# Kernel optimization log

Hardware: AMD Instinct MI355X
Metric: run time of the kernel (lower is better)

Reference implementation:

```python
import jax, jax.numpy as jnp
import numpy as np

IN_DIM, HIDDEN, NCLASS = 128, 512, 10
BETA, THRESH = 0.9, 0.15


def setup_inputs() -> dict:
    key = jax.random.key(0)
    k_x, k_w1, k_w2 = jax.random.split(key, 3)
    B, T = 512, 512
    x = jax.random.uniform(k_x, (B, T, IN_DIM), dtype=jnp.float32)
    # kaiming_normal_(nonlinearity='linear'): std = 1/sqrt(fan_in); fc1 then scaled by 0.8
    W1 = jax.random.normal(k_w1, (HIDDEN, IN_DIM), dtype=jnp.float32) * (0.8 / np.sqrt(IN_DIM))
    b1 = jnp.zeros((HIDDEN,), dtype=jnp.float32)
    W2 = jax.random.normal(k_w2, (NCLASS, HIDDEN), dtype=jnp.float32) * (1.0 / np.sqrt(HIDDEN))
    b2 = jnp.zeros((NCLASS,), dtype=jnp.float32)
    return {"x": x, "W1": W1, "b1": b1, "W2": W2, "b2": b2}


def reference(x, W1, b1, W2, b2):
    B, T, D = x.shape
    xs = jnp.transpose(2.0 * x, (1, 0, 2))  # [T, B, D]

    def step(carry, xt):
        mem, acc = carry
        cur = xt @ W1.T + b1                      # [B, H]
        reset = (mem > THRESH).astype(cur.dtype)  # spike from previous mem (snntorch order)
        mem = BETA * mem + cur - reset * THRESH   # subtract reset
        spk = (mem > THRESH).astype(cur.dtype)
        acc = acc + spk @ W2.T + b2               # [B, C]
        return (mem, acc), None

    mem0 = jnp.zeros((B, HIDDEN), dtype=jnp.float32)
    acc0 = jnp.zeros((B, NCLASS), dtype=jnp.float32)
    (_, acc), _ = jax.lax.scan(step, (mem0, acc0), xs)
    return acc / T
```

## Files before the change

kernel.cpp:

```cpp
#include <hip/hip_runtime.h>

#define IN_DIM  128
#define HIDDEN  512
#define NCLASS  10
#define TSTEPS  512
#define BATCH   512
#define BETA    0.9f
#define THRESH  0.15f

typedef __attribute__((ext_vector_type(8))) short bf16x8;
typedef __attribute__((ext_vector_type(4))) float f32x4;

__device__ __forceinline__ unsigned short f2bf_rne(float f) {
    unsigned int u = __float_as_uint(f);
    u += 0x7FFFu + ((u >> 16) & 1u);
    return (unsigned short)(u >> 16);
}
__device__ __forceinline__ float bf2f(unsigned short h) {
    return __uint_as_float(((unsigned int)h) << 16);
}

__device__ __forceinline__ bf16x8 cvt8(const float4 a, const float4 b, float s) {
    float v[8] = {a.x * s, a.y * s, a.z * s, a.w * s,
                  b.x * s, b.y * s, b.z * s, b.w * s};
    bf16x8 o;
#pragma unroll
    for (int e = 0; e < 8; ++e) o[e] = (short)f2bf_rne(v[e]);
    return o;
}

__device__ __forceinline__ void cvt8s(const float4 a, const float4 b,
                                      bf16x8* hi, bf16x8* lo) {
    float v[8] = {a.x, a.y, a.z, a.w, b.x, b.y, b.z, b.w};
#pragma unroll
    for (int e = 0; e < 8; ++e) {
        unsigned short h = f2bf_rne(v[e]);
        (*hi)[e] = (short)h;
        (*lo)[e] = (short)f2bf_rne(v[e] - bf2f(h));
    }
}

__global__ __launch_bounds__(256, 4) void conv_x3(
    const float* __restrict__ x, unsigned short* __restrict__ xt)
{
    const int bid  = blockIdx.x;
    const int bblk = bid >> 9;
    const int t    = bid & 511;
    const int g    = threadIdx.x;
    const int kf   = g >> 6;
    const int i    = g & 63;
    const int l15  = i & 15;
    const int lg   = i >> 4;

    const float* src = x + ((size_t)(bblk * 16 + l15) * TSTEPS + t) * IN_DIM
                         + kf * 32 + lg * 8;
    const float4* p = reinterpret_cast<const float4*>(src);
    unsigned short* tile = xt + ((size_t)bblk * TSTEPS + t) * 2048;
    *(bf16x8*)(tile + g * 8) = cvt8(p[0], p[1], 2.0f);
}

__global__ __launch_bounds__(256, 1) void snn_mfma_a(
    const unsigned short* __restrict__ xt,
    const float* __restrict__ W1, const float* __restrict__ b1,
    float* __restrict__ cnt_ws)
{
    __shared__ char ring[16][4096];

    const int bid  = blockIdx.x;
    const int hblk = bid >> 5;
    const int bblk = bid & 31;
    const int b0   = bblk * 16;
    const int tid  = threadIdx.x;
    const int wave = tid >> 6;
    const int lane = tid & 63;
    const int l15  = lane & 15;
    const int lg   = lane >> 4;
    const int hbase = hblk * 64 + wave * 16;

    bf16x8 whi[4], wlo[4];
    {
        const float* wp = W1 + (size_t)(hbase + l15) * IN_DIM + lg * 8;
#pragma unroll
        for (int kf = 0; kf < 4; ++kf) {
            const float4* p = reinterpret_cast<const float4*>(wp + kf * 32);
            cvt8s(p[0], p[1], &whi[kf], &wlo[kf]);
        }
    }
    const float b1h = b1[hbase + l15];

    const char* gb = (const char*)xt + (size_t)bblk * TSTEPS * 4096;
    char* lsb = &ring[0][0];
    const int woff   = wave * 1024;
    const int lane16 = lane * 16;
    const unsigned lbase =
        (unsigned)(unsigned long long)(__attribute__((address_space(3))) char*)&ring[0][0]
        + (unsigned)lane16;

    f32x4 mem = {0.f, 0.f, 0.f, 0.f}, cnt = {0.f, 0.f, 0.f, 0.f};

#define STAGE(TT)                                                              \
    {                                                                          \
        const char* g_ = gb + (size_t)(TT) * 4096 + woff + lane16;             \
        char* l_ = lsb + ((TT) & 15) * 4096 + woff;                            \
        __builtin_amdgcn_global_load_lds((const __attribute__((address_space(1))) void*)g_, (__attribute__((address_space(3))) void*)l_, 16, 0, 0); \
    }

#define RD1(OFF, DST)                                                          \
    asm volatile("ds_read_b128 %0, %1 offset:%c2"                              \
                 : "=&v"(DST) : "v"(lbase), "i"(OFF))

#define RD4A(S, F)                                                             \
    RD1((S) * 4096 + 0,    F[0]);                                              \
    RD1((S) * 4096 + 1024, F[1]);                                              \
    RD1((S) * 4096 + 2048, F[2]);                                              \
    RD1((S) * 4096 + 3072, F[3]);

#define MFMA_ACC(F, CH, CL)                                                    \
    CH = (f32x4){b1h, b1h, b1h, b1h};                                          \
    CL = (f32x4){0.f, 0.f, 0.f, 0.f};                                          \
    _Pragma("unroll")                                                          \
    for (int kf = 0; kf < 4; ++kf) {                                           \
        CH = __builtin_amdgcn_mfma_f32_16x16x32_bf16(F[kf], whi[kf], CH, 0, 0, 0); \
        CL = __builtin_amdgcn_mfma_f32_16x16x32_bf16(F[kf], wlo[kf], CL, 0, 0, 0); \
    }

#define REC(PH, PL)                                                            \
    _Pragma("unroll")                                                          \
    for (int r = 0; r < 4; ++r) {                                              \
        float cur = PH[r] + PL[r];                                             \
        float dec = fmaf(BETA, mem[r], cur);                                   \
        mem[r] = (mem[r] > THRESH) ? (dec - THRESH) : dec;                     \
        cnt[r] += (mem[r] > THRESH) ? 1.0f : 0.0f;                             \
    }

#define ITER_B(J, CF, NF, CH, CL, PH, PL)                                      \
    {                                                                          \
        asm volatile("s_waitcnt vmcnt(2)" ::: "memory");                       \
        __builtin_amdgcn_s_barrier();                                          \
        asm volatile("" ::: "memory");                                         \
        STAGE(tb + (J) + 7)                                                    \
        RD4A((tb + (J) + 1) & 15, NF)                                          \
        asm volatile("s_waitcnt lgkmcnt(4)" ::: "memory");                     \
        __builtin_amdgcn_sched_barrier(0);                                     \
        MFMA_ACC(CF, CH, CL)                                                   \
        REC(PH, PL)                                                            \
    }

#define ITER_N(J, CF, NF, CH, CL, PH, PL)                                      \
    {                                                                          \
        STAGE(tb + (J) + 7)                                                    \
        RD4A((tb + (J) + 1) & 15, NF)                                          \
        asm volatile("s_waitcnt lgkmcnt(4)" ::: "memory");                     \
        __builtin_amdgcn_sched_barrier(0);                                     \
        MFMA_ACC(CF, CH, CL)                                                   \
        REC(PH, PL)                                                            \
    }

    bf16x8 fA[4], fB[4];
    f32x4 hA, lA, hB, lB;
    hB = (f32x4){0.f, 0.f, 0.f, 0.f};
    lB = (f32x4){0.f, 0.f, 0.f, 0.f};

    asm volatile("s_waitcnt vmcnt(0)" ::: "memory");
#pragma unroll
    for (int j = 0; j < 7; ++j)
        STAGE(j)
    asm volatile("s_waitcnt vmcnt(6)" ::: "memory");
    __builtin_amdgcn_s_barrier();
    asm volatile("" ::: "memory");
    RD4A(0, fA)

    for (int w = 0; w < TSTEPS / 16; ++w) {
        const int tb = w * 16;
        ITER_B(0,  fA, fB, hA, lA, hB, lB)  ITER_N(1,  fB, fA, hB, lB, hA, lA)
        ITER_N(2,  fA, fB, hA, lA, hB, lB)  ITER_N(3,  fB, fA, hB, lB, hA, lA)
        ITER_B(4,  fA, fB, hA, lA, hB, lB)  ITER_N(5,  fB, fA, hB, lB, hA, lA)
        ITER_N(6,  fA, fB, hA, lA, hB, lB)  ITER_N(7,  fB, fA, hB, lB, hA, lA)
        ITER_B(8,  fA, fB, hA, lA, hB, lB)  ITER_N(9,  fB, fA, hB, lB, hA, lA)
        ITER_N(10, fA, fB, hA, lA, hB, lB)  ITER_N(11, fB, fA, hB, lB, hA, lA)
        ITER_B(12, fA, fB, hA, lA, hB, lB)  ITER_N(13, fB, fA, hB, lB, hA, lA)
        ITER_N(14, fA, fB, hA, lA, hB, lB)  ITER_N(15, fB, fA, hB, lB, hA, lA)
    }
    REC(hB, lB)
#undef ITER_B
#undef ITER_N
#undef REC
#undef MFMA_ACC
#undef RD4A
#undef RD1
#undef STAGE

    float* cp = cnt_ws + (size_t)b0 * HIDDEN + hbase + l15;
#pragma unroll
    for (int r = 0; r < 4; ++r)
        cp[(size_t)(lg * 4 + r) * HIDDEN] = cnt[r];
}

__global__ __launch_bounds__(256, 1) void snn_mfma_lds(
    const float* __restrict__ x, const float* __restrict__ W1,
    const float* __restrict__ b1, float* __restrict__ cnt_ws)
{
    __shared__ short ldsA[2][2][16 * IN_DIM];
    const int bid  = blockIdx.x;
    const int hblk = bid >> 5;
    const int bblk = bid & 31;
    const int b0   = bblk * 16;
    const int tid  = threadIdx.x;
    const int wave = tid >> 6;
    const int lane = tid & 63;
    const int l15  = lane & 15;
    const int lg   = lane >> 4;
    const int hbase = hblk * 64 + wave * 16;

    bf16x8 whi[4], wlo[4];
    {
        const float* wp = W1 + (size_t)(hbase + l15) * IN_DIM + lg * 8;
#pragma unroll
        for (int kf = 0; kf < 4; ++kf) {
            const float4* p = reinterpret_cast<const float4*>(wp + kf * 32);
            cvt8s(p[0], p[1], &whi[kf], &wlo[kf]);
        }
    }
    const float b1h = b1[hbase + l15];
    const int m_w  = wave * 4 + lg;
    const int widx = m_w * IN_DIM + ((l15 ^ (m_w & 7)) * 8);
    const float* xrow = x + ((size_t)(b0 + m_w) * TSTEPS) * IN_DIM + l15 * 8;
    int ridx[4];
#pragma unroll
    for (int kf = 0; kf < 4; ++kf)
        ridx[kf] = l15 * IN_DIM + (((lg + 4 * kf) ^ (l15 & 7)) * 8);

    f32x4 mem = {0.f, 0.f, 0.f, 0.f};
    f32x4 cnt = {0.f, 0.f, 0.f, 0.f};
    {
        const float4* p = reinterpret_cast<const float4*>(xrow);
        *(bf16x8*)&ldsA[0][0][widx] = cvt8(p[0], p[1], 2.0f);
    }
    float4 rA0, rA1, rB0, rB1;
    {
        const float4* p1 = reinterpret_cast<const float4*>(xrow + 1 * IN_DIM);
        rA0 = p1[0]; rA1 = p1[1];
        const float4* p2 = reinterpret_cast<const float4*>(xrow + 2 * IN_DIM);
        rB0 = p2[0]; rB1 = p2[1];
    }
    __syncthreads();

#define SNN_BODY(T_CUR, RC0, RC1)                                              \
    {                                                                          \
        const int buf = (T_CUR) & 1;                                           \
        if ((T_CUR) + 1 < TSTEPS) {                                            \
            *(bf16x8*)&ldsA[buf ^ 1][0][widx] = cvt8(RC0, RC1, 2.0f);          \
        }                                                                      \
        bf16x8 ahi[4];                                                         \
        _Pragma("unroll")                                                      \
        for (int kf = 0; kf < 4; ++kf)                                         \
            ahi[kf] = *(const bf16x8*)&ldsA[buf][0][ridx[kf]];                 \
        {                                                                      \
            int tld = (T_CUR) + 3;                                             \
            if (tld > TSTEPS - 1) tld = TSTEPS - 1;                            \
            const float4* p = reinterpret_cast<const float4*>(                 \
                xrow + (size_t)tld * IN_DIM);                                  \
            RC0 = p[0]; RC1 = p[1];                                            \
        }                                                                      \
        f32x4 chh = {b1h, b1h, b1h, b1h};                                      \
        f32x4 chl = {0.f, 0.f, 0.f, 0.f};                                      \
        _Pragma("unroll")                                                      \
        for (int kf = 0; kf < 4; ++kf) {                                       \
            chh = __builtin_amdgcn_mfma_f32_16x16x32_bf16(ahi[kf], whi[kf], chh, 0, 0, 0); \
            chl = __builtin_amdgcn_mfma_f32_16x16x32_bf16(ahi[kf], wlo[kf], chl, 0, 0, 0); \
        }                                                                      \
        _Pragma("unroll")                                                      \
        for (int r = 0; r < 4; ++r) {                                          \
            float cur = chh[r] + chl[r];                                       \
            float dec = fmaf(BETA, mem[r], cur);                               \
            mem[r] = (mem[r] > THRESH) ? (dec - THRESH) : dec;                 \
            cnt[r] += (mem[r] > THRESH) ? 1.0f : 0.0f;                         \
        }                                                                      \
        __syncthreads();                                                       \
    }

    for (int t = 0; t < TSTEPS; t += 2) {
        SNN_BODY(t,     rA0, rA1)
        SNN_BODY(t + 1, rB0, rB1)
    }
#undef SNN_BODY

    float* cp = cnt_ws + (size_t)b0 * HIDDEN + hbase + l15;
#pragma unroll
    for (int r = 0; r < 4; ++r)
        cp[(size_t)(lg * 4 + r) * HIDDEN] = cnt[r];
}

__global__ __launch_bounds__(64, 1) void snn_out(
    const float* __restrict__ cnt_ws, const float* __restrict__ W2,
    const float* __restrict__ b2, float* __restrict__ out)
{
    const int b = blockIdx.x;
    const int lane = threadIdx.x;
    float c8[8];
#pragma unroll
    for (int j = 0; j < 8; ++j)
        c8[j] = cnt_ws[(size_t)b * HIDDEN + lane + 64 * j];
#pragma unroll
    for (int c = 0; c < NCLASS; ++c) {
        float s = 0.f;
#pragma unroll
        for (int j = 0; j < 8; ++j)
            s = fmaf(c8[j], W2[c * HIDDEN + lane + 64 * j], s);
#pragma unroll
        for (int off = 32; off >= 1; off >>= 1)
            s += __shfl_xor(s, off, 64);
        if (lane == c)
            out[(size_t)b * NCLASS + c] = s * (1.0f / (float)TSTEPS) + b2[c];
    }
}

extern "C" void kernel_launch(void* const* d_in, const int* in_sizes, int n_in,
                              void* d_out, int out_size, void* d_ws, size_t ws_size,
                              hipStream_t stream) {
    const float* x  = (const float*)d_in[0];
    const float* W1 = (const float*)d_in[1];
    const float* b1 = (const float*)d_in[2];
    const float* W2 = (const float*)d_in[3];
    const float* b2 = (const float*)d_in[4];
    float* out = (float*)d_out;

    const size_t NX = (size_t)BATCH * TSTEPS * IN_DIM;
    float* cnt_ws = (float*)d_ws;
    unsigned short* xt = (unsigned short*)((char*)d_ws + (1u << 20));
    const size_t need = (1u << 20) + (NX + 8 * 2048) * sizeof(unsigned short);

    if (ws_size >= need) {
        conv_x3<<<dim3(32 * TSTEPS), dim3(256), 0, stream>>>(x, xt);
        snn_mfma_a<<<dim3(256), dim3(256), 0, stream>>>(xt, W1, b1, cnt_ws);
    } else {
        snn_mfma_lds<<<dim3(256), dim3(256), 0, stream>>>(x, W1, b1, cnt_ws);
    }
    snn_out<<<dim3(BATCH), dim3(64), 0, stream>>>(cnt_ws, W2, b2, out);
}
```

Measured before the change: 118.1 us.

## Process two timesteps per iteration with interleaved MFMA chains

Restructures the time loop so each step computes the input projection for two consecutive timesteps. It interleaves four independent MFMA accumulation chains, which hides MFMA dependency latency, and drops the one-step software pipeline of recurrence versus MFMA. Staging now runs 8 steps ahead, two loads per pair, and the ds_read double buffer grows to four fragment sets. This raises register pressure, and the recurrence now runs directly after the MFMAs of the same pair, which may expose their latency.

```diff
diff --git a/kernel.cpp b/kernel.cpp
--- a/kernel.cpp
+++ b/kernel.cpp
@@ -87,6 +87,8 @@
         }
     }
     const float b1h = b1[hbase + l15];
+    const f32x4 B1 = {b1h, b1h, b1h, b1h};
+    const f32x4 Z0 = {0.f, 0.f, 0.f, 0.f};
 
     const char* gb = (const char*)xt + (size_t)bblk * TSTEPS * 4096;
     char* lsb = &ring[0][0];
@@ -115,13 +117,17 @@
     RD1((S) * 4096 + 2048, F[2]);                                              \
     RD1((S) * 4096 + 3072, F[3]);
 
-#define MFMA_ACC(F, CH, CL)                                                    \
-    CH = (f32x4){b1h, b1h, b1h, b1h};                                          \
-    CL = (f32x4){0.f, 0.f, 0.f, 0.f};                                          \
+#define MFMA_PAIR(F0, F1, H0, L0, H1, L1)                                      \
+    H0 = __builtin_amdgcn_mfma_f32_16x16x32_bf16(F0[0], whi[0], B1, 0, 0, 0);  \
+    H1 = __builtin_amdgcn_mfma_f32_16x16x32_bf16(F1[0], whi[0], B1, 0, 0, 0);  \
+    L0 = __builtin_amdgcn_mfma_f32_16x16x32_bf16(F0[0], wlo[0], Z0, 0, 0, 0);  \
+    L1 = __builtin_amdgcn_mfma_f32_16x16x32_bf16(F1[0], wlo[0], Z0, 0, 0, 0);  \
     _Pragma("unroll")                                                          \
-    for (int kf = 0; kf < 4; ++kf) {                                           \
-        CH = __builtin_amdgcn_mfma_f32_16x16x32_bf16(F[kf], whi[kf], CH, 0, 0, 0); \
-        CL = __builtin_amdgcn_mfma_f32_16x16x32_bf16(F[kf], wlo[kf], CL, 0, 0, 0); \
+    for (int kf = 1; kf < 4; ++kf) {                                           \
+        H0 = __builtin_amdgcn_mfma_f32_16x16x32_bf16(F0[kf], whi[kf], H0, 0, 0, 0); \
+        H1 = __builtin_amdgcn_mfma_f32_16x16x32_bf16(F1[kf], whi[kf], H1, 0, 0, 0); \
+        L0 = __builtin_amdgcn_mfma_f32_16x16x32_bf16(F0[kf], wlo[kf], L0, 0, 0, 0); \
+        L1 = __builtin_amdgcn_mfma_f32_16x16x32_bf16(F1[kf], wlo[kf], L1, 0, 0, 0); \
     }
 
 #define REC(PH, PL)                                                            \
@@ -133,59 +139,59 @@
         cnt[r] += (mem[r] > THRESH) ? 1.0f : 0.0f;                             \
     }
 
-#define ITER_B(J, CF, NF, CH, CL, PH, PL)                                      \
+#define PAIR_B(J, CF0, CF1, NF0, NF1)                                          \
     {                                                                          \
         asm volatile("s_waitcnt vmcnt(2)" ::: "memory");                       \
         __builtin_amdgcn_s_barrier();                                          \
         asm volatile("" ::: "memory");                                         \
-        STAGE(tb + (J) + 7)                                                    \
-        RD4A((tb + (J) + 1) & 15, NF)                                          \
-        asm volatile("s_waitcnt lgkmcnt(4)" ::: "memory");                     \
+        STAGE(tb + 2 * (J) + 8)                                                \
+        STAGE(tb + 2 * (J) + 9)                                                \
+        RD4A((tb + 2 * (J) + 2) & 15, NF0)                                     \
+        RD4A((tb + 2 * (J) + 3) & 15, NF1)                                     \
+        asm volatile("s_waitcnt lgkmcnt(8)" ::: "memory");                     \
         __builtin_amdgcn_sched_barrier(0);                                     \
-        MFMA_ACC(CF, CH, CL)                                                   \
-        REC(PH, PL)                                                            \
-    }
-
-#define ITER_N(J, CF, NF, CH, CL, PH, PL)                                      \
+        MFMA_PAIR(CF0, CF1, hA, lA, hB, lB)                                    \
+        REC(hA, lA)                                                            \
+        REC(hB, lB)                                                            \
+    }
+
+#define PAIR_N(J, CF0, CF1, NF0, NF1)                                          \
     {                                                                          \
-        STAGE(tb + (J) + 7)                                                    \
-        RD4A((tb + (J) + 1) & 15, NF)                                          \
-        asm volatile("s_waitcnt lgkmcnt(4)" ::: "memory");                     \
+        STAGE(tb + 2 * (J) + 8)                                                \
+        STAGE(tb + 2 * (J) + 9)                                                \
+        RD4A((tb + 2 * (J) + 2) & 15, NF0)                                     \
+        RD4A((tb + 2 * (J) + 3) & 15, NF1)                                     \
+        asm volatile("s_waitcnt lgkmcnt(8)" ::: "memory");                     \
         __builtin_amdgcn_sched_barrier(0);                                     \
-        MFMA_ACC(CF, CH, CL)                                                   \
-        REC(PH, PL)                                                            \
-    }
-
-    bf16x8 fA[4], fB[4];
+        MFMA_PAIR(CF0, CF1, hA, lA, hB, lB)                                    \
+        REC(hA, lA)                                                            \
+        REC(hB, lB)                                                            \
+    }
+
+    bf16x8 fA[4], fB[4], fC[4], fD[4];
     f32x4 hA, lA, hB, lB;
-    hB = (f32x4){0.f, 0.f, 0.f, 0.f};
-    lB = (f32x4){0.f, 0.f, 0.f, 0.f};
 
     asm volatile("s_waitcnt vmcnt(0)" ::: "memory");
 #pragma unroll
-    for (int j = 0; j < 7; ++j)
+    for (int j = 0; j < 8; ++j)
         STAGE(j)
     asm volatile("s_waitcnt vmcnt(6)" ::: "memory");
     __builtin_amdgcn_s_barrier();
     asm volatile("" ::: "memory");
     RD4A(0, fA)
+    RD4A(1, fB)
 
     for (int w = 0; w < TSTEPS / 16; ++w) {
         const int tb = w * 16;
-        ITER_B(0,  fA, fB, hA, lA, hB, lB)  ITER_N(1,  fB, fA, hB, lB, hA, lA)
-        ITER_N(2,  fA, fB, hA, lA, hB, lB)  ITER_N(3,  fB, fA, hB, lB, hA, lA)
-        ITER_B(4,  fA, fB, hA, lA, hB, lB)  ITER_N(5,  fB, fA, hB, lB, hA, lA)
-        ITER_N(6,  fA, fB, hA, lA, hB, lB)  ITER_N(7,  fB, fA, hB, lB, hA, lA)
-        ITER_B(8,  fA, fB, hA, lA, hB, lB)  ITER_N(9,  fB, fA, hB, lB, hA, lA)
-        ITER_N(10, fA, fB, hA, lA, hB, lB)  ITER_N(11, fB, fA, hB, lB, hA, lA)
-        ITER_B(12, fA, fB, hA, lA, hB, lB)  ITER_N(13, fB, fA, hB, lB, hA, lA)
-        ITER_N(14, fA, fB, hA, lA, hB, lB)  ITER_N(15, fB, fA, hB, lB, hA, lA)
-    }
-    REC(hB, lB)
-#undef ITER_B
-#undef ITER_N
+        PAIR_B(0, fA, fB, fC, fD)  PAIR_N(1, fC, fD, fA, fB)
+        PAIR_B(2, fA, fB, fC, fD)  PAIR_N(3, fC, fD, fA, fB)
+        PAIR_B(4, fA, fB, fC, fD)  PAIR_N(5, fC, fD, fA, fB)
+        PAIR_B(6, fA, fB, fC, fD)  PAIR_N(7, fC, fD, fA, fB)
+    }
+#undef PAIR_B
+#undef PAIR_N
 #undef REC
-#undef MFMA_ACC
+#undef MFMA_PAIR
 #undef RD4A
 #undef RD1
 #undef STAGE
```

After: 116.8 us. About the same (-1.0%).
